# Kernel optimization log

Measured on AMD Instinct MI355X. Metric: run time of the kernel, lower is better.

The kernel has to match this reference:

```python
import jax, jax.numpy as jnp
import numpy as np

_EPS = 1e-12  # torch F.normalize eps


def _normalize(x):
    # x: [B, N, 3]; matches torch.nn.functional.normalize(x, dim=2)
    norm = jnp.linalg.norm(x, axis=2, keepdims=True)
    return x / jnp.maximum(norm, _EPS)


def setup_inputs() -> dict:
    key = jax.random.key(0)
    k1, k2 = jax.random.split(key)
    xyz1 = jax.random.normal(k1, (8, 4096, 6), dtype=jnp.float32)
    xyz2 = jax.random.normal(k2, (8, 4096, 6), dtype=jnp.float32)
    return {"xyz1": xyz1, "xyz2": xyz2}


def reference(xyz1, xyz2):
    p1 = xyz1[:, :, :3]  # [B, N, 3]
    p2 = xyz2[:, :, :3]  # [B, M, 3]
    n1 = xyz1[:, :, 3:]  # [B, N, 3]
    n2 = xyz2[:, :, 3:]  # [B, M, 3]

    # Pairwise squared L2: |a|^2 + |b|^2 - 2 a.b  -> [B, N, M]
    sq1 = jnp.sum(p1 * p1, axis=2)  # [B, N]
    sq2 = jnp.sum(p2 * p2, axis=2)  # [B, M]
    cross = jnp.einsum('bnd,bmd->bnm', p1, p2)
    d = sq1[:, :, None] + sq2[:, None, :] - 2.0 * cross  # [B, N, M]

    dist1 = jnp.min(d, axis=2)      # [B, N] NN of each p1 in p2
    idx1 = jnp.argmin(d, axis=2)    # [B, N]
    dist2 = jnp.min(d, axis=1)      # [B, M] NN of each p2 in p1
    idx2 = jnp.argmin(d, axis=1)    # [B, M]

    # Gather matched normals
    t1 = jnp.take_along_axis(n2, idx1[:, :, None], axis=1)  # [B, N, 3]
    t2 = jnp.take_along_axis(n1, idx2[:, :, None], axis=1)  # [B, M, 3]

    nd1 = jnp.sum((_normalize(n1) - _normalize(t1)) ** 2, axis=2)  # [B, N]
    nd2 = jnp.sum((_normalize(n2) - _normalize(t2)) ** 2, axis=2)  # [B, M]

    return jnp.mean(dist1) + jnp.mean(dist2) + jnp.mean(nd1) + jnp.mean(nd2)
```

## Files before the change

kernel.cpp:

```cpp
#include <hip/hip_runtime.h>
#include <cstdint>

#define NB 8
#define NP 4096

typedef __attribute__((ext_vector_type(8))) short bf16x8;
typedef __attribute__((ext_vector_type(4))) float f32x4;
typedef __attribute__((ext_vector_type(4))) unsigned int u32x4;


__device__ inline void split3(float x, unsigned short& a, unsigned short& b,
                              unsigned short& c) {
    unsigned int xb = __float_as_uint(x);
    float s0 = __uint_as_float(xb & 0xFFFF0000u);
    float r1 = x - s0;
    unsigned int r1b = __float_as_uint(r1);
    float s1 = __uint_as_float(r1b & 0xFFFF0000u);
    float r2 = r1 - s1;
    unsigned int r2b = __float_as_uint(r2);
    a = (unsigned short)(xb >> 16);
    b = (unsigned short)(r1b >> 16);
    c = (unsigned short)(r2b >> 16);
}

__global__ __launch_bounds__(256) void chamfer_prep(
    const float* __restrict__ xyz1, const float* __restrict__ xyz2,
    unsigned int* __restrict__ atab, float* __restrict__ out)
{
    int gid = blockIdx.x * 256 + threadIdx.x;
    if (gid == 0) out[0] = 0.0f;
    int pt  = gid & (NP - 1);
    int b   = (gid >> 12) & 7;
    int set = gid >> 15;

    const float* src = (set ? xyz2 : xyz1) + ((size_t)b * NP + pt) * 6;
    float x = src[0], y = src[1], z = src[2];

    unsigned short sx[3], sy[3], sz[3], sb[3];
    split3(x, sx[0], sx[1], sx[2]);
    split3(y, sy[0], sy[1], sy[2]);
    split3(z, sz[0], sz[1], sz[2]);
    float bias = 0.5f * (x * x + y * y + z * z);
    split3(bias, sb[0], sb[1], sb[2]);

    unsigned short S[32];
    #pragma unroll
    for (int d = 0; d < 3; ++d) {
        #pragma unroll
        for (int i = 0; i < 3; ++i) {
            unsigned short v = (d == 0 ? sx[i] : (d == 1 ? sy[i] : sz[i]));
            v ^= 0x8000;
            #pragma unroll
            for (int j = 0; j < 3; ++j) S[d * 9 + i * 3 + j] = v;
        }
    }
    S[27] = sb[0]; S[28] = sb[1]; S[29] = sb[2];
    S[30] = 0x3F80; S[31] = 0x3F80;

    u32x4* dst = reinterpret_cast<u32x4*>(atab + (size_t)gid * 16);
    #pragma unroll
    for (int m = 0; m < 4; ++m) {
        u32x4 w;
        #pragma unroll
        for (int e = 0; e < 4; ++e) {
            int k = m * 8 + e * 2;
            w[e] = (unsigned int)S[k] | ((unsigned int)S[k + 1] << 16);
        }
        dst[m] = w;
    }
}

__device__ inline void gload_lds16(const unsigned int* g, unsigned int* l) {
    __builtin_amdgcn_global_load_lds(
        (const __attribute__((address_space(1))) unsigned int*)g,
        (__attribute__((address_space(3))) unsigned int*)l, 16, 0, 0);
}

__global__ __launch_bounds__(256) void chamfer_mfma(
    const float* __restrict__ xyz1, const float* __restrict__ xyz2,
    const unsigned int* __restrict__ atab, unsigned int* __restrict__ part)
{
    __shared__ unsigned int stage[8192];

    int bx    = blockIdx.x;
    int thalf = bx & 1;
    int qc    = (bx >> 1) & 31;
    int b     = (bx >> 6) & 7;
    int dir   = bx >> 9;

    const float* qset = dir ? xyz2 : xyz1;
    int tid = threadIdx.x;
    int w   = tid >> 6;
    int l   = tid & 63;
    int col = l & 15;
    int g   = l >> 4;

    if (tid < 128) {
        const float* qs = qset + ((size_t)b * NP + qc * 128 + tid) * 6;
        float qx = qs[0], qy = qs[1], qz = qs[2];
        unsigned short sx[3], sy[3], sz[3];
        split3(qx, sx[0], sx[1], sx[2]);
        split3(qy, sy[0], sy[1], sy[2]);
        split3(qz, sz[0], sz[1], sz[2]);
        float qq2 = 0.5f * (qx * qx + qy * qy + qz * qz);
        unsigned int qqb = __float_as_uint(qq2);
        float qh = __uint_as_float(qqb & 0xFFFF0000u);
        unsigned int qlb = __float_as_uint(qq2 - qh);

        unsigned short S[32];
        #pragma unroll
        for (int d = 0; d < 3; ++d)
            #pragma unroll
            for (int i = 0; i < 3; ++i)
                #pragma unroll
                for (int j = 0; j < 3; ++j)
                    S[d * 9 + i * 3 + j] =
                        (d == 0 ? sx[j] : (d == 1 ? sy[j] : sz[j]));
        S[27] = 0x3F80; S[28] = 0x3F80; S[29] = 0x3F80;
        S[30] = (unsigned short)(qqb >> 16);
        S[31] = (unsigned short)(qlb >> 16);
        #pragma unroll
        for (int m = 0; m < 16; ++m)
            stage[tid * 16 + m] =
                (unsigned int)S[2 * m] | ((unsigned int)S[2 * m + 1] << 16);
    }
    __syncthreads();
    bf16x8 bf0 = *reinterpret_cast<const bf16x8*>(&stage[(w * 32 + col) * 16 + g * 4]);
    bf16x8 bf1 = *reinterpret_cast<const bf16x8*>(&stage[(w * 32 + 16 + col) * 16 + g * 4]);
    __syncthreads();

    const unsigned int* abase =
        atab + ((size_t)((1 - dir) * NB + b) * NP + thalf * 2048) * 16;

    unsigned int p0r = 0xFFFFFFFFu, p1r = 0xFFFFFFFFu;
    unsigned int vX = (unsigned int)(g * 4);
    f32x4 czero = {0.0f, 0.0f, 0.0f, 0.0f};

    for (int s0 = 0; s0 < 2048; s0 += 512) {
        const unsigned int* src = abase + (size_t)s0 * 16;
        #pragma unroll
        for (int r = 0; r < 8; ++r)
            gload_lds16(src + r * 1024 + tid * 4, &stage[r * 1024 + tid * 4]);
        __syncthreads();

        #pragma unroll 4
        for (int t = 0; t < 32; ++t) {
            bf16x8 af = *reinterpret_cast<const bf16x8*>(
                &stage[(t * 16 + col) * 16 + g * 4]);
            f32x4 D0 = __builtin_amdgcn_mfma_f32_16x16x32_bf16(af, bf0, czero, 0, 0, 0);
            f32x4 D1 = __builtin_amdgcn_mfma_f32_16x16x32_bf16(af, bf1, czero, 0, 0, 0);
            unsigned int a0 = (__float_as_uint(D0[0]) & 0xFFFFF000u);
            unsigned int a1 = (__float_as_uint(D0[1]) & 0xFFFFF000u) | 1u;
            unsigned int a2 = (__float_as_uint(D0[2]) & 0xFFFFF000u) | 2u;
            unsigned int a3 = (__float_as_uint(D0[3]) & 0xFFFFF000u) | 3u;
            unsigned int pm0 = min(min(a0, a1), min(a2, a3));
            p0r = min(p0r, pm0 | vX);
            unsigned int c0 = (__float_as_uint(D1[0]) & 0xFFFFF000u);
            unsigned int c1 = (__float_as_uint(D1[1]) & 0xFFFFF000u) | 1u;
            unsigned int c2 = (__float_as_uint(D1[2]) & 0xFFFFF000u) | 2u;
            unsigned int c3 = (__float_as_uint(D1[3]) & 0xFFFFF000u) | 3u;
            unsigned int pm1 = min(min(c0, c1), min(c2, c3));
            p1r = min(p1r, pm1 | vX);
            vX += 16u;
        }
        __syncthreads();
    }

    p0r = min(p0r, (unsigned int)__shfl_xor((int)p0r, 16, 64));
    p0r = min(p0r, (unsigned int)__shfl_xor((int)p0r, 32, 64));
    p1r = min(p1r, (unsigned int)__shfl_xor((int)p1r, 16, 64));
    p1r = min(p1r, (unsigned int)__shfl_xor((int)p1r, 32, 64));

    if (l < 32) {
        unsigned int val = (l < 16) ? p0r : p1r;
        part[(size_t)thalf * (2 * NB * NP) +
             ((size_t)(dir * NB + b) * NP) + qc * 128 + w * 32 + l] = val;
    }
}

__global__ __launch_bounds__(256) void chamfer_finish(
    const float* __restrict__ xyz1, const float* __restrict__ xyz2,
    const unsigned int* __restrict__ part, float* __restrict__ out)
{
    int gid = blockIdx.x * 256 + threadIdx.x;
    int q   = gid & (NP - 1);
    int db  = gid >> 12;
    int b   = db & 7;
    int dir = db >> 3;

    unsigned int p0 = part[gid];
    unsigned int p1 = part[2 * NB * NP + gid];
    int seg = (p1 < p0) ? 1 : 0;
    unsigned int p = seg ? p1 : p0;

    const float* qset = dir ? xyz2 : xyz1;
    const float* tset = dir ? xyz1 : xyz2;

    float dist = fmaxf(2.0f * __uint_as_float(p & 0xFFFFF000u), 0.0f);
    int j = seg * 2048 + (int)(p & 0xFFFu);

    const float* nq = qset + ((size_t)b * NP + q) * 6 + 3;
    const float* nt = tset + ((size_t)b * NP + j) * 6 + 3;
    float ax = nq[0], ay = nq[1], az = nq[2];
    float bx = nt[0], by = nt[1], bz = nt[2];

    float na = fmaxf(sqrtf(ax * ax + ay * ay + az * az), 1e-12f);
    float nb = fmaxf(sqrtf(bx * bx + by * by + bz * bz), 1e-12f);
    float ra = 1.0f / na, rb = 1.0f / nb;
    float dx = ax * ra - bx * rb;
    float dy = ay * ra - by * rb;
    float dz = az * ra - bz * rb;
    float nd = dx * dx + dy * dy + dz * dz;

    float contrib = (dist + nd) * (1.0f / 32768.0f);

    for (int off = 32; off > 0; off >>= 1)
        contrib += __shfl_down(contrib, off, 64);
    __shared__ float wsum[4];
    if ((threadIdx.x & 63) == 0) wsum[threadIdx.x >> 6] = contrib;
    __syncthreads();
    if (threadIdx.x == 0)
        atomicAdd(out, wsum[0] + wsum[1] + wsum[2] + wsum[3]);
}

extern "C" void kernel_launch(void* const* d_in, const int* in_sizes, int n_in,
                              void* d_out, int out_size, void* d_ws, size_t ws_size,
                              hipStream_t stream) {
    const float* xyz1 = (const float*)d_in[0];
    const float* xyz2 = (const float*)d_in[1];
    float* out = (float*)d_out;

    unsigned int* part = (unsigned int*)d_ws;
    unsigned int* atab = part + 2 * (2 * NB * NP);

    chamfer_prep<<<256, 256, 0, stream>>>(xyz1, xyz2, atab, out);
    chamfer_mfma<<<1024, 256, 0, stream>>>(xyz1, xyz2, atab, part);
    chamfer_finish<<<(2 * NB * NP) / 256, 256, 0, stream>>>(xyz1, xyz2, part, out);
}
```

Measured before the change: 92.89 us.

## Widen per-block query tile to 256 and split targets into quarters with swizzled LDS

Each block now handles 256 query points instead of 128, so each wave runs four MFMAs per loaded A fragment instead of two. The target range per block shrinks from half to a quarter, which keeps the grid at 1024 blocks. The LDS layout of the staged target table is swizzled to cut bank conflicts, and the finish kernel now reduces four partials per query instead of two. Each loaded target tile is reused more, at the cost of more live registers and a larger partials buffer.

```diff
diff --git a/kernel.cpp b/kernel.cpp
--- a/kernel.cpp
+++ b/kernel.cpp
@@ -82,11 +82,11 @@
 {
     __shared__ unsigned int stage[8192];
 
-    int bx    = blockIdx.x;
-    int thalf = bx & 1;
-    int qc    = (bx >> 1) & 31;
-    int b     = (bx >> 6) & 7;
-    int dir   = bx >> 9;
+    int bx  = blockIdx.x;
+    int tq  = bx & 3;
+    int qc  = (bx >> 2) & 15;
+    int b   = (bx >> 6) & 7;
+    int dir = bx >> 9;
 
     const float* qset = dir ? xyz2 : xyz1;
     int tid = threadIdx.x;
@@ -95,8 +95,8 @@
     int col = l & 15;
     int g   = l >> 4;
 
-    if (tid < 128) {
-        const float* qs = qset + ((size_t)b * NP + qc * 128 + tid) * 6;
+    {
+        const float* qs = qset + ((size_t)b * NP + qc * 256 + tid) * 6;
         float qx = qs[0], qy = qs[1], qz = qs[2];
         unsigned short sx[3], sy[3], sz[3];
         split3(qx, sx[0], sx[1], sx[2]);
@@ -125,57 +125,70 @@
                 (unsigned int)S[2 * m] | ((unsigned int)S[2 * m + 1] << 16);
     }
     __syncthreads();
-    bf16x8 bf0 = *reinterpret_cast<const bf16x8*>(&stage[(w * 32 + col) * 16 + g * 4]);
-    bf16x8 bf1 = *reinterpret_cast<const bf16x8*>(&stage[(w * 32 + 16 + col) * 16 + g * 4]);
+    bf16x8 bf0 = *reinterpret_cast<const bf16x8*>(&stage[(w * 64 +  0 + col) * 16 + g * 4]);
+    bf16x8 bf1 = *reinterpret_cast<const bf16x8*>(&stage[(w * 64 + 16 + col) * 16 + g * 4]);
+    bf16x8 bf2 = *reinterpret_cast<const bf16x8*>(&stage[(w * 64 + 32 + col) * 16 + g * 4]);
+    bf16x8 bf3 = *reinterpret_cast<const bf16x8*>(&stage[(w * 64 + 48 + col) * 16 + g * 4]);
     __syncthreads();
 
     const unsigned int* abase =
-        atab + ((size_t)((1 - dir) * NB + b) * NP + thalf * 2048) * 16;
-
-    unsigned int p0r = 0xFFFFFFFFu, p1r = 0xFFFFFFFFu;
-    unsigned int vX = (unsigned int)(g * 4);
+        atab + ((size_t)((1 - dir) * NB + b) * NP + tq * 1024) * 16;
+
+    unsigned int p0 = 0xFFFFFFFFu, p1 = 0xFFFFFFFFu;
+    unsigned int p2 = 0xFFFFFFFFu, p3 = 0xFFFFFFFFu;
+    unsigned int vx0 = (unsigned int)(g * 4 + 0);
+    unsigned int vx1 = (unsigned int)(g * 4 + 1);
+    unsigned int vx2 = (unsigned int)(g * 4 + 2);
+    unsigned int vx3 = (unsigned int)(g * 4 + 3);
     f32x4 czero = {0.0f, 0.0f, 0.0f, 0.0f};
-
-    for (int s0 = 0; s0 < 2048; s0 += 512) {
+    const unsigned int MSK = 0xFFFFF000u;
+    int swz = (g + (col >> 1)) & 3;
+
+    for (int s0 = 0; s0 < 1024; s0 += 512) {
         const unsigned int* src = abase + (size_t)s0 * 16;
         #pragma unroll
-        for (int r = 0; r < 8; ++r)
-            gload_lds16(src + r * 1024 + tid * 4, &stage[r * 1024 + tid * 4]);
+        for (int r = 0; r < 8; ++r) {
+            int R = r * 64 + (tid >> 2);
+            int c = ((tid & 3) - ((tid >> 3) & 3)) & 3;
+            gload_lds16(src + (size_t)R * 16 + c * 4,
+                        &stage[r * 1024 + tid * 4]);
+        }
         __syncthreads();
 
-        #pragma unroll 4
+        #pragma unroll 2
         for (int t = 0; t < 32; ++t) {
             bf16x8 af = *reinterpret_cast<const bf16x8*>(
-                &stage[(t * 16 + col) * 16 + g * 4]);
+                &stage[(t * 16 + col) * 16 + swz * 4]);
             f32x4 D0 = __builtin_amdgcn_mfma_f32_16x16x32_bf16(af, bf0, czero, 0, 0, 0);
             f32x4 D1 = __builtin_amdgcn_mfma_f32_16x16x32_bf16(af, bf1, czero, 0, 0, 0);
-            unsigned int a0 = (__float_as_uint(D0[0]) & 0xFFFFF000u);
-            unsigned int a1 = (__float_as_uint(D0[1]) & 0xFFFFF000u) | 1u;
-            unsigned int a2 = (__float_as_uint(D0[2]) & 0xFFFFF000u) | 2u;
-            unsigned int a3 = (__float_as_uint(D0[3]) & 0xFFFFF000u) | 3u;
-            unsigned int pm0 = min(min(a0, a1), min(a2, a3));
-            p0r = min(p0r, pm0 | vX);
-            unsigned int c0 = (__float_as_uint(D1[0]) & 0xFFFFF000u);
-            unsigned int c1 = (__float_as_uint(D1[1]) & 0xFFFFF000u) | 1u;
-            unsigned int c2 = (__float_as_uint(D1[2]) & 0xFFFFF000u) | 2u;
-            unsigned int c3 = (__float_as_uint(D1[3]) & 0xFFFFF000u) | 3u;
-            unsigned int pm1 = min(min(c0, c1), min(c2, c3));
-            p1r = min(p1r, pm1 | vX);
-            vX += 16u;
+            f32x4 D2 = __builtin_amdgcn_mfma_f32_16x16x32_bf16(af, bf2, czero, 0, 0, 0);
+            f32x4 D3 = __builtin_amdgcn_mfma_f32_16x16x32_bf16(af, bf3, czero, 0, 0, 0);
+            #define PACK(P, D) do {                                          \
+                unsigned int a0 = (__float_as_uint((D)[0]) & MSK) | vx0;     \
+                unsigned int a1 = (__float_as_uint((D)[1]) & MSK) | vx1;     \
+                unsigned int a2 = (__float_as_uint((D)[2]) & MSK) | vx2;     \
+                unsigned int a3 = (__float_as_uint((D)[3]) & MSK) | vx3;     \
+                P = min(P, min(min(a0, a1), min(a2, a3)));                   \
+            } while (0)
+            PACK(p0, D0); PACK(p1, D1); PACK(p2, D2); PACK(p3, D3);
+            #undef PACK
+            vx0 += 16u; vx1 += 16u; vx2 += 16u; vx3 += 16u;
         }
         __syncthreads();
     }
 
-    p0r = min(p0r, (unsigned int)__shfl_xor((int)p0r, 16, 64));
-    p0r = min(p0r, (unsigned int)__shfl_xor((int)p0r, 32, 64));
-    p1r = min(p1r, (unsigned int)__shfl_xor((int)p1r, 16, 64));
-    p1r = min(p1r, (unsigned int)__shfl_xor((int)p1r, 32, 64));
-
-    if (l < 32) {
-        unsigned int val = (l < 16) ? p0r : p1r;
-        part[(size_t)thalf * (2 * NB * NP) +
-             ((size_t)(dir * NB + b) * NP) + qc * 128 + w * 32 + l] = val;
-    }
+    p0 = min(p0, (unsigned int)__shfl_xor((int)p0, 16, 64));
+    p0 = min(p0, (unsigned int)__shfl_xor((int)p0, 32, 64));
+    p1 = min(p1, (unsigned int)__shfl_xor((int)p1, 16, 64));
+    p1 = min(p1, (unsigned int)__shfl_xor((int)p1, 32, 64));
+    p2 = min(p2, (unsigned int)__shfl_xor((int)p2, 16, 64));
+    p2 = min(p2, (unsigned int)__shfl_xor((int)p2, 32, 64));
+    p3 = min(p3, (unsigned int)__shfl_xor((int)p3, 16, 64));
+    p3 = min(p3, (unsigned int)__shfl_xor((int)p3, 32, 64));
+
+    unsigned int val = (g < 2) ? (g == 0 ? p0 : p1) : (g == 2 ? p2 : p3);
+    part[(size_t)tq * (2 * NB * NP) +
+         ((size_t)(dir * NB + b) * NP) + qc * 256 + w * 64 + l] = val;
 }
 
 __global__ __launch_bounds__(256) void chamfer_finish(
@@ -188,16 +201,20 @@
     int b   = db & 7;
     int dir = db >> 3;
 
-    unsigned int p0 = part[gid];
-    unsigned int p1 = part[2 * NB * NP + gid];
-    int seg = (p1 < p0) ? 1 : 0;
-    unsigned int p = seg ? p1 : p0;
+    unsigned int c0 = part[gid];
+    unsigned int c1 = part[1 * (2 * NB * NP) + gid];
+    unsigned int c2 = part[2 * (2 * NB * NP) + gid];
+    unsigned int c3 = part[3 * (2 * NB * NP) + gid];
+    unsigned int best = c0; int qs = 0;
+    if (c1 < best) { best = c1; qs = 1; }
+    if (c2 < best) { best = c2; qs = 2; }
+    if (c3 < best) { best = c3; qs = 3; }
 
     const float* qset = dir ? xyz2 : xyz1;
     const float* tset = dir ? xyz1 : xyz2;
 
-    float dist = fmaxf(2.0f * __uint_as_float(p & 0xFFFFF000u), 0.0f);
-    int j = seg * 2048 + (int)(p & 0xFFFu);
+    float dist = fmaxf(2.0f * __uint_as_float(best & 0xFFFFF000u), 0.0f);
+    int j = qs * 1024 + (int)(best & 0xFFFu);
 
     const float* nq = qset + ((size_t)b * NP + q) * 6 + 3;
     const float* nt = tset + ((size_t)b * NP + j) * 6 + 3;
@@ -231,7 +248,7 @@
     float* out = (float*)d_out;
 
     unsigned int* part = (unsigned int*)d_ws;
-    unsigned int* atab = part + 2 * (2 * NB * NP);
+    unsigned int* atab = part + 4 * (2 * NB * NP);
 
     chamfer_prep<<<256, 256, 0, stream>>>(xyz1, xyz2, atab, out);
     chamfer_mfma<<<1024, 256, 0, stream>>>(xyz1, xyz2, atab, part);
```

Measured after the change: 91.30 us. Within noise of the previous version (-1.7%).
